# Performance work log

Hardware: AMD Instinct MI355X
Metric: run time of the kernel (lower is better)

## Reference

```python
import jax, jax.numpy as jnp
import numpy as np

N_HEAD, D_K = 16, 64  # from init_kwargs (d_v == d_k)

def setup_inputs() -> dict:
    key = jax.random.key(0)
    ks = jax.random.split(key, 8)
    B, S, D, DFF = 8, 1024, 1024, 4096
    s = 1.0 / np.sqrt(D)
    return {
        "enc_input": jax.random.normal(ks[0], (B, S, D), jnp.float32),
        "mask": jnp.ones((B, 1, S), jnp.int32),
        "gap": 1,
        "wq": jax.random.normal(ks[1], (D, N_HEAD * D_K), jnp.float32) * s,
        "wk": jax.random.normal(ks[2], (D, N_HEAD * D_K), jnp.float32) * s,
        "wv": jax.random.normal(ks[3], (D, N_HEAD * D_K), jnp.float32) * s,
        "wo": jax.random.normal(ks[4], (N_HEAD * D_K, D), jnp.float32) * s,
        "w1": jax.random.normal(ks[5], (D, DFF), jnp.float32) * s,
        "b1": jnp.zeros((DFF,), jnp.float32),
        "w2": jax.random.normal(ks[6], (DFF, D), jnp.float32) * (1.0 / np.sqrt(DFF)),
        "b2": jnp.zeros((D,), jnp.float32),
    }

def reference(enc_input, mask, gap, wq, wk, wv, wo, w1, b1, w2, b2):
    # dropout=0, use_layer_norm=0, adapter=0 are hard-coded in EncoderLayer.__init__
    B, S, D = enc_input.shape
    H, dk = N_HEAD, D_K
    temperature = dk ** 0.5

    q = (enc_input @ wq).reshape(B, S, H, dk).transpose(0, 2, 1, 3)  # [B,H,S,dk]
    k = (enc_input @ wk).reshape(B, S, H, dk).transpose(0, 2, 1, 3)
    v = (enc_input @ wv).reshape(B, S, H, dk).transpose(0, 2, 1, 3)

    attn = jnp.einsum('bhqd,bhkd->bhqk', q / temperature, k)  # [B,H,S,S]
    # mask [B,1,S] -> unsqueeze head dim -> [B,1,1,S]
    attn = jnp.where(mask[:, None] == 0, jnp.float32(-1e9), attn)
    attn = jax.nn.softmax(attn, axis=-1)

    ctx = jnp.einsum('bhqk,bhkd->bhqd', attn, v)          # [B,H,S,dk]
    ctx = ctx.transpose(0, 2, 1, 3).reshape(B, S, H * dk)  # [B,S,D]
    enc = ctx @ wo + enc_input                              # attn residual

    ffn = jax.nn.relu(enc @ w1 + b1) @ w2 + b2
    out = ffn + enc                                         # ffn residual
    return out, attn
```

## Files before the change

kernel.cpp:

```cpp
#include <hip/hip_runtime.h>
#include <hip/hip_bf16.h>
#include <stdint.h>

typedef __bf16 bf16x8 __attribute__((ext_vector_type(8)));
typedef float  f32x4  __attribute__((ext_vector_type(4)));

typedef __attribute__((address_space(1))) void gvoid;
typedef __attribute__((address_space(3))) void lvoid;

__device__ __forceinline__ void async16(void* lds, const void* g) {
    __builtin_amdgcn_global_load_lds((gvoid*)g, (lvoid*)lds, 16, 0, 0);
}

__device__ __forceinline__ float fexp2(float x) {
    return __builtin_amdgcn_exp2f(x);
}

__global__ void prep_all(const float* __restrict__ X, __hip_bfloat16* __restrict__ Xb,
                         const float* __restrict__ wq, const float* __restrict__ wk,
                         const float* __restrict__ wv, const float* __restrict__ wo,
                         const float* __restrict__ w1, const float* __restrict__ w2,
                         __hip_bfloat16* __restrict__ Wcat,
                         __hip_bfloat16* __restrict__ Wot,
                         __hip_bfloat16* __restrict__ W1t,
                         __hip_bfloat16* __restrict__ W2t) {
    const int tix = blockIdx.x;
    if (tix >= 12288) {
        const int bi = tix - 12288;
        const int tid = threadIdx.y * 32 + threadIdx.x;
        const long i = ((long)bi * 256 + tid) * 4;
        float4 v = *(const float4*)(X + i);
        __hip_bfloat162* d = (__hip_bfloat162*)(Xb + i);
        d[0] = __float22bfloat162_rn(make_float2(v.x, v.y));
        d[1] = __float22bfloat162_rn(make_float2(v.z, v.w));
        return;
    }
    __shared__ float t[32][33];
    const float* in;
    __hip_bfloat16* out;
    int R, C, cx, cy;
    if (tix < 4096) {
        int wid = tix >> 10, tile = tix & 1023;
        const float* srcs[4] = {wq, wk, wv, wo};
        __hip_bfloat16* dsts[4] = {Wcat, Wcat + 1024 * 1024, Wcat + 2 * 1024 * 1024, Wot};
        in = srcs[wid]; out = dsts[wid];
        R = 1024; C = 1024; cx = tile & 31; cy = tile >> 5;
    } else if (tix < 8192) {
        int tile = tix - 4096;
        in = w1; out = W1t; R = 1024; C = 4096;
        cx = tile & 127; cy = tile >> 7;
    } else {
        int tile = tix - 8192;
        in = w2; out = W2t; R = 4096; C = 1024;
        cx = tile & 31; cy = tile >> 5;
    }
    const int c0 = cx * 32, r0 = cy * 32;
    const int tx = threadIdx.x, ty = threadIdx.y;
#pragma unroll
    for (int i = 0; i < 4; ++i) {
        int r = r0 + ty + i * 8;
        t[ty + i * 8][tx] = in[(long)r * C + c0 + tx];
    }
    __syncthreads();
#pragma unroll
    for (int i = 0; i < 4; ++i) {
        int c = c0 + ty + i * 8;
        out[(long)c * R + r0 + tx] = __float2bfloat16(t[tx][ty + i * 8]);
    }
}

#define RBAR asm volatile("s_barrier" ::: "memory")

__global__ void __launch_bounds__(256, 2)
attn_fused(const __hip_bfloat16* __restrict__ QKb,
           const __hip_bfloat16* __restrict__ Vt,
           const int* __restrict__ mask,
           float* __restrict__ attn,
           __hip_bfloat16* __restrict__ Ctx) {
    __shared__ __align__(16) __hip_bfloat16 sK[128 * 64];
    __shared__ __align__(16) __hip_bfloat16 sV[64 * 128];
    __shared__ __align__(16) __hip_bfloat16 sP[128 * 128];
    __shared__ float smadd[1024];

    const int tid = threadIdx.x, lane = tid & 63, wave = tid >> 6;
    const int r16 = lane & 15, kg = lane >> 4;
    const float SC2 = 0.125f * 1.44269504f;

    const int dd = blockIdx.x;
    const int wgt = (dd & 7) * 128 + (dd >> 3);
    const int xblk = wgt & 7, z = wgt >> 3;
    const int b = z >> 4, h = z & 15;
    const int row0 = xblk * 128;
    const int wrow = wave * 32;

    const __hip_bfloat16* Qz = QKb + ((long)b * 1024 + row0) * 2048 + h * 64;
    const __hip_bfloat16* Kz = QKb + (long)b * 1024 * 2048 + 1024 + h * 64;
    const __hip_bfloat16* Vz = Vt + (long)z * 64 * 1024;
    float* attnZ = attn + (long)z * 1024 * 1024 + (long)row0 * 1024;

    for (int i = tid; i < 1024; i += 256)
        smadd[i] = mask[b * 1024 + i] ? 0.f : -1.5e9f;

    bf16x8 qa[2][2];
#pragma unroll
    for (int m = 0; m < 2; ++m)
#pragma unroll
        for (int kf = 0; kf < 2; ++kf)
            qa[m][kf] = *(const bf16x8*)(Qz + (long)(wrow + m * 16 + r16) * 2048 + kf * 32 + kg * 8);

    float lrow[2][4];
#pragma unroll
    for (int m = 0; m < 2; ++m)
#pragma unroll
        for (int i = 0; i < 4; ++i) lrow[m][i] = 0.f;

    const int ssw = (r16 & 7) << 4;

    auto stageK = [&](char* dst, int ct) {
#pragma unroll
        for (int j = 0; j < 4; ++j) {
            int c = wave * 4 + j;
            int s = c * 8 + (lane >> 3);
            int cb = (lane & 7) * 16;
            async16(dst + c * 1024,
                    (const char*)(Kz + (long)(ct * 128 + s) * 2048) + (cb ^ ((s & 7) << 4)));
        }
    };
    auto stageV = [&](int ct) {
#pragma unroll
        for (int j = 0; j < 4; ++j) {
            int c = wave * 4 + j;
            int dv = c * 4 + (lane >> 4);
            int cb = (lane & 15) * 16;
            async16((char*)sV + c * 1024,
                    (const char*)(Vz + (long)dv * 1024 + ct * 128) + (cb ^ ((dv & 7) << 4)));
        }
    };

    char* kbuf0 = (char*)sK;
    char* kbuf1 = (char*)sP;
    stageK(kbuf0, 0);

    for (int ct = 0; ct < 8; ++ct) {
        asm volatile("s_waitcnt vmcnt(0)" ::: "memory");
        __syncthreads();
        if (ct < 7) stageK((ct & 1) ? kbuf0 : kbuf1, ct + 1);
        const char* base = (ct & 1) ? kbuf1 : kbuf0;

        f32x4 sacc[2][8];
#pragma unroll
        for (int m = 0; m < 2; ++m)
#pragma unroll
            for (int nf = 0; nf < 8; ++nf) sacc[m][nf] = f32x4{0.f, 0.f, 0.f, 0.f};

        __builtin_amdgcn_s_setprio(1);
#pragma unroll
        for (int nf = 0; nf < 8; ++nf) {
            const char* kr = base + (nf * 16 + r16) * 128;
            bf16x8 bv0 = *(const bf16x8*)(kr + ((kg * 16) ^ ssw));
            bf16x8 bv1 = *(const bf16x8*)(kr + ((64 + kg * 16) ^ ssw));
#pragma unroll
            for (int m = 0; m < 2; ++m) {
                sacc[m][nf] = __builtin_amdgcn_mfma_f32_16x16x32_bf16(qa[m][0], bv0, sacc[m][nf], 0, 0, 0);
                sacc[m][nf] = __builtin_amdgcn_mfma_f32_16x16x32_bf16(qa[m][1], bv1, sacc[m][nf], 0, 0, 0);
            }
        }
        __builtin_amdgcn_s_setprio(0);

        float madd[8];
#pragma unroll
        for (int nf = 0; nf < 8; ++nf) madd[nf] = smadd[ct * 128 + nf * 16 + r16];

#pragma unroll
        for (int m = 0; m < 2; ++m)
#pragma unroll
            for (int i = 0; i < 4; ++i) {
                float ts = 0.f;
#pragma unroll
                for (int nf = 0; nf < 8; ++nf)
                    ts += fexp2(sacc[m][nf][i] * SC2 + madd[nf]);
#pragma unroll
                for (int o = 1; o < 16; o <<= 1) ts += __shfl_xor(ts, o);
                lrow[m][i] += ts;
            }
    }

    float rinv[2][4];
#pragma unroll
    for (int m = 0; m < 2; ++m)
#pragma unroll
        for (int i = 0; i < 4; ++i) rinv[m][i] = 1.0f / lrow[m][i];

    f32x4 oacc[2][4];
#pragma unroll
    for (int m = 0; m < 2; ++m)
#pragma unroll
        for (int nf = 0; nf < 4; ++nf) oacc[m][nf] = f32x4{0.f, 0.f, 0.f, 0.f};

    __syncthreads();
    stageK((char*)sK, 0);
    stageV(0);

    for (int ct = 0; ct < 8; ++ct) {
        asm volatile("s_waitcnt vmcnt(0)" ::: "memory");
        __syncthreads();

        f32x4 sacc[2][8];
#pragma unroll
        for (int m = 0; m < 2; ++m)
#pragma unroll
            for (int nf = 0; nf < 8; ++nf) sacc[m][nf] = f32x4{0.f, 0.f, 0.f, 0.f};

        __builtin_amdgcn_s_setprio(1);
#pragma unroll
        for (int nf = 0; nf < 8; ++nf) {
            const char* kr = (const char*)sK + (nf * 16 + r16) * 128;
            bf16x8 bv0 = *(const bf16x8*)(kr + ((kg * 16) ^ ssw));
            bf16x8 bv1 = *(const bf16x8*)(kr + ((64 + kg * 16) ^ ssw));
#pragma unroll
            for (int m = 0; m < 2; ++m) {
                sacc[m][nf] = __builtin_amdgcn_mfma_f32_16x16x32_bf16(qa[m][0], bv0, sacc[m][nf], 0, 0, 0);
                sacc[m][nf] = __builtin_amdgcn_mfma_f32_16x16x32_bf16(qa[m][1], bv1, sacc[m][nf], 0, 0, 0);
            }
        }
        __builtin_amdgcn_s_setprio(0);

        RBAR;
        if (ct < 7) stageK((char*)sK, ct + 1);

        float madd[8];
#pragma unroll
        for (int nf = 0; nf < 8; ++nf) madd[nf] = smadd[ct * 128 + nf * 16 + r16];

#pragma unroll
        for (int m = 0; m < 2; ++m)
#pragma unroll
            for (int nf = 0; nf < 8; ++nf) {
                int scol = nf * 16 + r16;
#pragma unroll
                for (int i = 0; i < 4; ++i) {
                    int q = wrow + m * 16 + kg * 4 + i;
                    float p = fexp2(sacc[m][nf][i] * SC2 + madd[nf]) * rinv[m][i];
                    __builtin_nontemporal_store(p, attnZ + (long)q * 1024 + ct * 128 + scol);
                    *(__hip_bfloat16*)((char*)sP + q * 256 + ((scol * 2) ^ ((q & 7) << 4))) =
                        __float2bfloat16(p);
                }
            }

        __builtin_amdgcn_s_setprio(1);
#pragma unroll
        for (int ks = 0; ks < 4; ++ks) {
            bf16x8 pa[2], vv[4];
#pragma unroll
            for (int m = 0; m < 2; ++m)
                pa[m] = *(const bf16x8*)((const char*)sP + (wrow + m * 16 + r16) * 256 +
                                         ((ks * 64 + kg * 16) ^ ssw));
#pragma unroll
            for (int nf = 0; nf < 4; ++nf)
                vv[nf] = *(const bf16x8*)((const char*)sV + (nf * 16 + r16) * 256 +
                                          ((ks * 64 + kg * 16) ^ ssw));
#pragma unroll
            for (int m = 0; m < 2; ++m)
#pragma unroll
                for (int nf = 0; nf < 4; ++nf)
                    oacc[m][nf] = __builtin_amdgcn_mfma_f32_16x16x32_bf16(pa[m], vv[nf], oacc[m][nf], 0, 0, 0);
        }
        __builtin_amdgcn_s_setprio(0);

        RBAR;
        if (ct < 7) stageV(ct + 1);
    }

#pragma unroll
    for (int m = 0; m < 2; ++m)
#pragma unroll
        for (int nf = 0; nf < 4; ++nf)
#pragma unroll
            for (int i = 0; i < 4; ++i) {
                int q = wrow + m * 16 + kg * 4 + i;
                Ctx[((long)b * 1024 + row0 + q) * 1024 + h * 64 + nf * 16 + r16] =
                    __float2bfloat16(oacc[m][nf][i]);
            }
}

#define RDA(BUF, PM, ML, KS) \
    (*(const bf16x8*)(aRd + (BUF)*32768 + (PM)*16384 + (ML)*2048 + ((((KS)*64) + kg*16) ^ sw)))
#define RDB(BUF, PN, NL, KS) \
    (*(const bf16x8*)(bRd + (BUF)*32768 + (PN)*16384 + (NL)*2048 + ((((KS)*64) + kg*16) ^ sw)))
#define LOAD_A(BUF, PM)                          \
    _Pragma("unroll") for (int ml = 0; ml < 4; ++ml) \
    _Pragma("unroll") for (int ks = 0; ks < 2; ++ks) \
        a[ml][ks] = RDA(BUF, PM, ml, ks)
#define LOAD_B(DST, BUF, PN)                     \
    _Pragma("unroll") for (int nl = 0; nl < 2; ++nl) \
    _Pragma("unroll") for (int ks = 0; ks < 2; ++ks) \
        DST[nl][ks] = RDB(BUF, PN, nl, ks)
#define MFMA16(PM, PN, BB)                                                   \
    __builtin_amdgcn_s_setprio(1);                                           \
    _Pragma("unroll") for (int ks = 0; ks < 2; ++ks)                         \
    _Pragma("unroll") for (int ml = 0; ml < 4; ++ml)                         \
    _Pragma("unroll") for (int nl = 0; nl < 2; ++nl)                         \
        acc[(PM)*4 + ml][(PN)*2 + nl] = __builtin_amdgcn_mfma_f32_16x16x32_bf16( \
            a[ml][ks], BB[nl][ks], acc[(PM)*4 + ml][(PN)*2 + nl], 0, 0, 0);  \
    __builtin_amdgcn_s_setprio(0)
#define BAR asm volatile("s_barrier" ::: "memory")

__global__ void __launch_bounds__(512, 2)
gemm256(const __hip_bfloat16* __restrict__ A, int lda,
        const __hip_bfloat16* __restrict__ Bt, int ldb,
        int K, int Mtiles,
        const float* __restrict__ bias, int relu,
        __hip_bfloat16* __restrict__ C, int ldc) {
    __shared__ __align__(16) char lds[131072];
    const int NT = K >> 6;
    const int tid = threadIdx.x, lane = tid & 63, wave = tid >> 6;
    const int r16 = lane & 15, kg = lane >> 4;
    const int wr = wave >> 2, wc = wave & 3;
    const int sw = (r16 & 7) << 4;

    const int nwg = gridDim.x;
    const int q8 = nwg >> 3, r8 = nwg & 7;
    const int xcd = blockIdx.x & 7, rest = blockIdx.x >> 3;
    const int wg = (xcd < r8 ? xcd * (q8 + 1) : r8 * (q8 + 1) + (xcd - r8) * q8) + rest;
    const int tm = wg % Mtiles, tn = wg / Mtiles;
    const long row0 = (long)tm * 256, col0 = (long)tn * 256;

    const int idx = tid >> 3;
    const int slotp = ((tid & 7) ^ (idx & 7)) * 8;
    const __hip_bfloat16* aSrc[4];
    const __hip_bfloat16* bSrc[4];
#pragma unroll
    for (int j = 0; j < 4; ++j) {
        long ar = row0 + (j & 1) * 128 + (j >> 1) * 64 + idx;
        aSrc[j] = A + ar * lda + slotp;
        long br = col0 + ((j & 1) * 2 + (tid >> 8)) * 64 + (j >> 1) * 32 + (idx & 31);
        bSrc[j] = Bt + br * ldb + slotp;
    }

    char* ldsA = lds;
    char* ldsB = lds + 65536;
    const int stDst = wave * 1024;
    auto stA = [&](int v, int j) {
        async16(ldsA + ((v & 1) << 15) + (j << 13) + stDst, aSrc[j] + (v << 6));
    };
    auto stB = [&](int v, int j) {
        async16(ldsB + ((v & 1) << 15) + (j << 13) + stDst, bSrc[j] + (v << 6));
    };

    stA(0, 0); stA(0, 1); stB(0, 0); stB(0, 1);
    stA(0, 2); stA(0, 3); stB(0, 2); stB(0, 3);
    stA(1, 0); stA(1, 1); stB(1, 0); stB(1, 1);
    asm volatile("s_waitcnt vmcnt(4)" ::: "memory");
    BAR;

    f32x4 acc[8][4] = {};
    const char* aRd = ldsA + wr * 8192 + r16 * 128;
    const char* bRd = ldsB + wc * 4096 + r16 * 128;

    for (int u = 0; u < NT; u += 2) {
        const bool more = (u + 2) < NT;
        bf16x8 a[4][2], b0[2][2], b1[2][2];

        LOAD_A(0, 0);
        LOAD_B(b0, 0, 0);
        stA(u + 1, 2); stA(u + 1, 3);
        MFMA16(0, 0, b0);
        BAR;

        LOAD_B(b1, 0, 1);
        stB(u + 1, 2); stB(u + 1, 3);
        MFMA16(0, 1, b1);
        BAR;

        LOAD_A(0, 1);
        if (more) { stA(u + 2, 0); stA(u + 2, 1); }
        MFMA16(1, 0, b0);
        BAR;

        if (more) {
            stB(u + 2, 0); stB(u + 2, 1);
            asm volatile("s_waitcnt vmcnt(4)" ::: "memory");
        } else {
            asm volatile("s_waitcnt vmcnt(0)" ::: "memory");
        }
        MFMA16(1, 1, b1);
        BAR;

        LOAD_A(1, 0);
        LOAD_B(b0, 1, 0);
        if (more) { stA(u + 2, 2); stA(u + 2, 3); }
        MFMA16(0, 0, b0);
        BAR;

        LOAD_B(b1, 1, 1);
        if (more) { stB(u + 2, 2); stB(u + 2, 3); }
        MFMA16(0, 1, b1);
        BAR;

        LOAD_A(1, 1);
        if (more) { stA(u + 3, 0); stA(u + 3, 1); }
        MFMA16(1, 0, b0);
        BAR;

        if (more) {
            stB(u + 3, 0); stB(u + 3, 1);
            asm volatile("s_waitcnt vmcnt(4)" ::: "memory");
        }
        MFMA16(1, 1, b1);
        BAR;
    }

    const long crow = row0 + wr * 128, ccol = col0 + wc * 64;
#pragma unroll
    for (int mf = 0; mf < 8; ++mf)
#pragma unroll
        for (int nf = 0; nf < 4; ++nf) {
            const long col = ccol + nf * 16 + r16;
            const float bs = bias ? bias[col] : 0.f;
#pragma unroll
            for (int i = 0; i < 4; ++i) {
                const long row = crow + mf * 16 + kg * 4 + i;
                float v = acc[mf][nf][i] + bs;
                if (relu) v = fmaxf(v, 0.f);
                C[row * (long)ldc + col] = __float2bfloat16(v);
            }
        }
}

#define RDB128(BUF, NL, KS) \
    (*(const bf16x8*)(bRd + (BUF)*16384 + (NL)*2048 + ((((KS)*64) + kg*16) ^ sw)))
#define LOAD_B128(DST, BUF)                      \
    _Pragma("unroll") for (int nl = 0; nl < 2; ++nl) \
    _Pragma("unroll") for (int ks = 0; ks < 2; ++ks) \
        DST[nl][ks] = RDB128(BUF, nl, ks)
#define MFMA16N(PM, BB)                                                      \
    __builtin_amdgcn_s_setprio(1);                                           \
    _Pragma("unroll") for (int ks = 0; ks < 2; ++ks)                         \
    _Pragma("unroll") for (int ml = 0; ml < 4; ++ml)                         \
    _Pragma("unroll") for (int nl = 0; nl < 2; ++nl)                         \
        acc[(PM)*4 + ml][nl] = __builtin_amdgcn_mfma_f32_16x16x32_bf16(      \
            a[ml][ks], BB[nl][ks], acc[(PM)*4 + ml][nl], 0, 0, 0);           \
    __builtin_amdgcn_s_setprio(0)

__global__ void __launch_bounds__(512, 2)
gemm256n128(const __hip_bfloat16* __restrict__ A, int lda,
            const __hip_bfloat16* __restrict__ Bt, int ldb,
            int K, int Mtiles,
            const float* __restrict__ bias, int relu,
            const float* __restrict__ resf,
            const __hip_bfloat16* __restrict__ resb, int ldres,
            float* __restrict__ Cf, __hip_bfloat16* __restrict__ Cb, int ldc) {
    __shared__ __align__(16) char lds[98304];
    const int NT = K >> 6;
    const int tid = threadIdx.x, lane = tid & 63, wave = tid >> 6;
    const int r16 = lane & 15, kg = lane >> 4;
    const int wr = wave >> 2, wc = wave & 3;
    const int sw = (r16 & 7) << 4;

    const int nwg = gridDim.x;
    const int q8 = nwg >> 3, r8 = nwg & 7;
    const int xcd = blockIdx.x & 7, rest = blockIdx.x >> 3;
    const int wg = (xcd < r8 ? xcd * (q8 + 1) : r8 * (q8 + 1) + (xcd - r8) * q8) + rest;
    const int tm = wg % Mtiles, tn = wg / Mtiles;
    const long row0 = (long)tm * 256, col0 = (long)tn * 128;

    const int idx = tid >> 3;
    const int slotp = ((tid & 7) ^ (idx & 7)) * 8;
    const __hip_bfloat16* aSrc[4];
    const __hip_bfloat16* bSrc[2];
#pragma unroll
    for (int j = 0; j < 4; ++j) {
        long ar = row0 + (j & 1) * 128 + (j >> 1) * 64 + idx;
        aSrc[j] = A + ar * lda + slotp;
    }
#pragma unroll
    for (int j = 0; j < 2; ++j) {
        long br = col0 + j * 64 + idx;
        bSrc[j] = Bt + br * ldb + slotp;
    }

    char* ldsA = lds;
    char* ldsB = lds + 65536;
    const int stDst = wave * 1024;
    auto stA = [&](int v, int j) {
        async16(ldsA + ((v & 1) << 15) + (j << 13) + stDst, aSrc[j] + (v << 6));
    };
    auto stB = [&](int v, int j) {
        async16(ldsB + ((v & 1) << 14) + (j << 13) + stDst, bSrc[j] + (v << 6));
    };

    stA(0, 0); stA(0, 1); stA(0, 2); stA(0, 3);
    stB(0, 0); stB(0, 1);
    stA(1, 0); stA(1, 1);
    stB(1, 0); stB(1, 1);
    asm volatile("s_waitcnt vmcnt(4)" ::: "memory");
    BAR;

    f32x4 acc[8][2] = {};
    const char* aRd = ldsA + wr * 8192 + r16 * 128;
    const char* bRd = ldsB + wc * 4096 + r16 * 128;

    for (int u = 0; u < NT; u += 2) {
        const bool more = (u + 2) < NT;
        bf16x8 a[4][2], b0[2][2], b1[2][2];

        LOAD_A(0, 0);
        LOAD_B128(b0, 0);
        stA(u + 1, 2); stA(u + 1, 3);
        MFMA16N(0, b0);
        BAR;

        LOAD_A(0, 1);
        if (more) {
            stA(u + 2, 0); stA(u + 2, 1);
            stB(u + 2, 0); stB(u + 2, 1);
            asm volatile("s_waitcnt vmcnt(4)" ::: "memory");
        } else {
            asm volatile("s_waitcnt vmcnt(0)" ::: "memory");
        }
        MFMA16N(1, b0);
        BAR;

        LOAD_A(1, 0);
        LOAD_B128(b1, 1);
        if (more) { stA(u + 2, 2); stA(u + 2, 3); }
        MFMA16N(0, b1);
        BAR;

        LOAD_A(1, 1);
        if (more) {
            stA(u + 3, 0); stA(u + 3, 1);
            stB(u + 3, 0); stB(u + 3, 1);
            asm volatile("s_waitcnt vmcnt(4)" ::: "memory");
        }
        MFMA16N(1, b1);
        BAR;
    }

    const long crow = row0 + wr * 128, ccol = col0 + wc * 32;
#pragma unroll
    for (int mf = 0; mf < 8; ++mf)
#pragma unroll
        for (int nf = 0; nf < 2; ++nf) {
            const long col = ccol + nf * 16 + r16;
            const float bs = bias ? bias[col] : 0.f;
#pragma unroll
            for (int i = 0; i < 4; ++i) {
                const long row = crow + mf * 16 + kg * 4 + i;
                float v = acc[mf][nf][i] + bs;
                if (relu) v = fmaxf(v, 0.f);
                if (resf) v += resf[row * (long)ldres + col];
                if (resb) v += __bfloat162float(resb[row * (long)ldres + col]);
                const long off = row * (long)ldc + col;
                if (Cf) Cf[off] = v;
                if (Cb) Cb[off] = __float2bfloat16(v);
            }
        }
}

__global__ void __launch_bounds__(512, 2)
gemm_v(const __hip_bfloat16* __restrict__ A, int lda,
       const __hip_bfloat16* __restrict__ Bt, int ldb,
       int K,
       __hip_bfloat16* __restrict__ Vt) {
    __shared__ __align__(16) char lds[98304];
    const int NT = K >> 6;
    const int tid = threadIdx.x, lane = tid & 63, wave = tid >> 6;
    const int r16 = lane & 15, kg = lane >> 4;
    const int wr = wave >> 2, wc = wave & 3;
    const int sw = (r16 & 7) << 4;

    const int nwg = gridDim.x;
    const int q8 = nwg >> 3, r8 = nwg & 7;
    const int xcd = blockIdx.x & 7, rest = blockIdx.x >> 3;
    const int wg = (xcd < r8 ? xcd * (q8 + 1) : r8 * (q8 + 1) + (xcd - r8) * q8) + rest;
    const int tm = wg & 31, tn = wg >> 5;
    const long row0 = (long)tm * 256, col0 = (long)tn * 128;

    const int idx = tid >> 3;
    const int slotp = ((tid & 7) ^ (idx & 7)) * 8;
    const __hip_bfloat16* aSrc[4];
    const __hip_bfloat16* bSrc[2];
#pragma unroll
    for (int j = 0; j < 4; ++j) {
        long ar = row0 + (j & 1) * 128 + (j >> 1) * 64 + idx;
        aSrc[j] = A + ar * lda + slotp;
    }
#pragma unroll
    for (int j = 0; j < 2; ++j) {
        long br = col0 + j * 64 + idx;
        bSrc[j] = Bt + br * ldb + slotp;
    }

    char* ldsA = lds;
    char* ldsB = lds + 65536;
    const int stDst = wave * 1024;
    auto stA = [&](int v, int j) {
        async16(ldsA + ((v & 1) << 15) + (j << 13) + stDst, aSrc[j] + (v << 6));
    };
    auto stB = [&](int v, int j) {
        async16(ldsB + ((v & 1) << 14) + (j << 13) + stDst, bSrc[j] + (v << 6));
    };

    stA(0, 0); stA(0, 1); stA(0, 2); stA(0, 3);
    stB(0, 0); stB(0, 1);
    stA(1, 0); stA(1, 1);
    stB(1, 0); stB(1, 1);
    asm volatile("s_waitcnt vmcnt(4)" ::: "memory");
    BAR;

    f32x4 acc[8][2] = {};
    const char* aRd = ldsA + wr * 8192 + r16 * 128;
    const char* bRd = ldsB + wc * 4096 + r16 * 128;

    for (int u = 0; u < NT; u += 2) {
        const bool more = (u + 2) < NT;
        bf16x8 a[4][2], b0[2][2], b1[2][2];

        LOAD_A(0, 0);
        LOAD_B128(b0, 0);
        stA(u + 1, 2); stA(u + 1, 3);
        MFMA16N(0, b0);
        BAR;

        LOAD_A(0, 1);
        if (more) {
            stA(u + 2, 0); stA(u + 2, 1);
            stB(u + 2, 0); stB(u + 2, 1);
            asm volatile("s_waitcnt vmcnt(4)" ::: "memory");
        } else {
            asm volatile("s_waitcnt vmcnt(0)" ::: "memory");
        }
        MFMA16N(1, b0);
        BAR;

        LOAD_A(1, 0);
        LOAD_B128(b1, 1);
        if (more) { stA(u + 2, 2); stA(u + 2, 3); }
        MFMA16N(0, b1);
        BAR;

        LOAD_A(1, 1);
        if (more) {
            stA(u + 3, 0); stA(u + 3, 1);
            stB(u + 3, 0); stB(u + 3, 1);
            asm volatile("s_waitcnt vmcnt(4)" ::: "memory");
        }
        MFMA16N(1, b1);
        BAR;
    }

    __hip_bfloat16* sT = (__hip_bfloat16*)lds;
    {
        const int cls = wc * 32;
        const int rls = wr * 128 + kg * 4;
#pragma unroll
        for (int mf = 0; mf < 8; ++mf)
#pragma unroll
            for (int nf = 0; nf < 2; ++nf) {
                int cl = cls + nf * 16 + r16;
                int rl = rls + mf * 16;
                __hip_bfloat162 lo = __float22bfloat162_rn(make_float2(acc[mf][nf][0], acc[mf][nf][1]));
                __hip_bfloat162 hi = __float22bfloat162_rn(make_float2(acc[mf][nf][2], acc[mf][nf][3]));
                *(__hip_bfloat162*)(&sT[cl * 264 + rl]) = lo;
                *(__hip_bfloat162*)(&sT[cl * 264 + rl + 2]) = hi;
            }
    }
    __syncthreads();
    {
        const int b = (int)(row0 >> 10);
        const int s_base = (int)(row0 & 1023);
#pragma unroll
        for (int j = 0; j < 8; ++j) {
            int dl = wave * 16 + j * 2 + (lane >> 5);
            int sc = (lane & 31) * 8;
            bf16x8 v = *(const bf16x8*)(&sT[dl * 264 + sc]);
            int dg = (int)col0 + dl;
            int z = b * 16 + (dg >> 6);
            int d = dg & 63;
            *(bf16x8*)(Vt + ((long)z * 64 + d) * 1024 + s_base + sc) = v;
        }
    }
}

extern "C" void kernel_launch(void* const* d_in, const int* in_sizes, int n_in,
                              void* d_out, int out_size, void* d_ws, size_t ws_size,
                              hipStream_t stream) {
    const int B = 8, S = 1024, D = 1024, DFF = 4096;
    const long SD = (long)B * S * D;

    const float* X  = (const float*)d_in[0];
    const int*  msk = (const int*)d_in[1];
    const float* wq = (const float*)d_in[3];
    const float* wk = (const float*)d_in[4];
    const float* wv = (const float*)d_in[5];
    const float* wo = (const float*)d_in[6];
    const float* w1 = (const float*)d_in[7];
    const float* b1 = (const float*)d_in[8];
    const float* w2 = (const float*)d_in[9];
    const float* b2 = (const float*)d_in[10];

    float* out  = (float*)d_out;
    float* attn = out + SD;

    char* ws = (char*)d_ws;
    auto alloc = [&](size_t bytes) {
        char* p = ws;
        ws += (bytes + 255) & ~(size_t)255;
        return p;
    };
    __hip_bfloat16* Xb   = (__hip_bfloat16*)alloc(SD * 2);
    __hip_bfloat16* QKb  = (__hip_bfloat16*)alloc(SD * 4);
    __hip_bfloat16* Vt   = (__hip_bfloat16*)alloc(SD * 2);
    __hip_bfloat16* Ctx  = (__hip_bfloat16*)alloc(SD * 2);
    __hip_bfloat16* EncB = (__hip_bfloat16*)alloc(SD * 2);
    __hip_bfloat16* Hb   = (__hip_bfloat16*)alloc((long)B * S * DFF * 2);
    __hip_bfloat16* Wcat = (__hip_bfloat16*)alloc((long)3 * D * D * 2);
    __hip_bfloat16* Wot  = (__hip_bfloat16*)alloc((long)D * D * 2);
    __hip_bfloat16* W1t  = (__hip_bfloat16*)alloc((long)D * DFF * 2);
    __hip_bfloat16* W2t  = (__hip_bfloat16*)alloc((long)D * DFF * 2);
    (void)ws_size; (void)in_sizes; (void)n_in; (void)out_size;

    dim3 tb(32, 8);
    prep_all<<<dim3(12288 + 8192), tb, 0, stream>>>(X, Xb, wq, wk, wv, wo, w1, w2,
                                                    Wcat, Wot, W1t, W2t);

    gemm256<<<dim3(32 * 8), 512, 0, stream>>>(
        Xb, D, Wcat, D, D, 32, nullptr, 0, QKb, 2048);

    gemm_v<<<dim3(32 * 8), 512, 0, stream>>>(
        Xb, D, Wcat + (long)2048 * 1024, D, D, Vt);

    attn_fused<<<dim3(1024), 256, 0, stream>>>(QKb, Vt, msk, attn, Ctx);

    gemm256n128<<<dim3(32 * 8), 512, 0, stream>>>(
        Ctx, D, Wot, D, D, 32,
        nullptr, 0, X, nullptr, D,
        nullptr, EncB, D);

    gemm256<<<dim3(32 * 16), 512, 0, stream>>>(
        EncB, D, W1t, D, D, 32, b1, 1, Hb, DFF);

    gemm256n128<<<dim3(32 * 8), 512, 0, stream>>>(
        Hb, DFF, W2t, DFF, DFF, 32,
        b2, 0, nullptr, EncB, D,
        out, nullptr, D);
}
```

Measured before the change: 510.4 us.

## Double-buffer V tiles and split P×V into halves in the attention pass

The second attention pass now double-buffers the V tile in LDS and issues the next K and V loads together, right after the QK^T MFMAs. The softmax-write and P·V step is split into two halves, so the P staging buffer shrinks to half its size and one loop-top barrier goes away. The goal is to overlap V loading with the exponent/store work and to cut synchronisation per tile. The end-of-iteration wait is only vmcnt(63), which may not guarantee the prefetched tiles have landed, especially with many outstanding nontemporal stores. That makes correctness depend on timing.

```diff
diff --git a/kernel.cpp b/kernel.cpp
--- a/kernel.cpp
+++ b/kernel.cpp
@@ -78,8 +78,8 @@
            float* __restrict__ attn,
            __hip_bfloat16* __restrict__ Ctx) {
     __shared__ __align__(16) __hip_bfloat16 sK[128 * 64];
-    __shared__ __align__(16) __hip_bfloat16 sV[64 * 128];
-    __shared__ __align__(16) __hip_bfloat16 sP[128 * 128];
+    __shared__ __align__(16) __hip_bfloat16 sV[2][64 * 128];
+    __shared__ __align__(16) __hip_bfloat16 sP[128 * 64];
     __shared__ float smadd[1024];
 
     const int tid = threadIdx.x, lane = tid & 63, wave = tid >> 6;
@@ -126,13 +126,13 @@
                     (const char*)(Kz + (long)(ct * 128 + s) * 2048) + (cb ^ ((s & 7) << 4)));
         }
     };
-    auto stageV = [&](int ct) {
+    auto stageV = [&](int ct, int buf) {
 #pragma unroll
         for (int j = 0; j < 4; ++j) {
             int c = wave * 4 + j;
             int dv = c * 4 + (lane >> 4);
             int cb = (lane & 15) * 16;
-            async16((char*)sV + c * 1024,
+            async16((char*)sV[buf] + c * 1024,
                     (const char*)(Vz + (long)dv * 1024 + ct * 128) + (cb ^ ((dv & 7) << 4)));
         }
     };
@@ -199,12 +199,11 @@
 
     __syncthreads();
     stageK((char*)sK, 0);
-    stageV(0);
+    stageV(0, 0);
+    asm volatile("s_waitcnt vmcnt(0)" ::: "memory");
+    __syncthreads();
 
     for (int ct = 0; ct < 8; ++ct) {
-        asm volatile("s_waitcnt vmcnt(0)" ::: "memory");
-        __syncthreads();
-
         f32x4 sacc[2][8];
 #pragma unroll
         for (int m = 0; m < 2; ++m)
@@ -226,49 +225,63 @@
         __builtin_amdgcn_s_setprio(0);
 
         RBAR;
-        if (ct < 7) stageK((char*)sK, ct + 1);
+        if (ct < 7) {
+            stageK((char*)sK, ct + 1);
+            stageV(ct + 1, (ct + 1) & 1);
+        }
+        asm volatile("" ::: "memory");
 
         float madd[8];
 #pragma unroll
         for (int nf = 0; nf < 8; ++nf) madd[nf] = smadd[ct * 128 + nf * 16 + r16];
 
-#pragma unroll
-        for (int m = 0; m < 2; ++m)
-#pragma unroll
-            for (int nf = 0; nf < 8; ++nf) {
-                int scol = nf * 16 + r16;
-#pragma unroll
-                for (int i = 0; i < 4; ++i) {
-                    int q = wrow + m * 16 + kg * 4 + i;
-                    float p = fexp2(sacc[m][nf][i] * SC2 + madd[nf]) * rinv[m][i];
-                    __builtin_nontemporal_store(p, attnZ + (long)q * 1024 + ct * 128 + scol);
-                    *(__hip_bfloat16*)((char*)sP + q * 256 + ((scol * 2) ^ ((q & 7) << 4))) =
-                        __float2bfloat16(p);
+        const char* sVb = (const char*)sV[ct & 1];
+
+#pragma unroll
+        for (int half = 0; half < 2; ++half) {
+#pragma unroll
+            for (int m = 0; m < 2; ++m)
+#pragma unroll
+                for (int nf = 0; nf < 4; ++nf) {
+                    const int nfg = half * 4 + nf;
+                    const int scol = nfg * 16 + r16;
+                    const int scl = nf * 16 + r16;
+#pragma unroll
+                    for (int i = 0; i < 4; ++i) {
+                        int q = wrow + m * 16 + kg * 4 + i;
+                        float p = fexp2(sacc[m][nfg][i] * SC2 + madd[nfg]) * rinv[m][i];
+                        __builtin_nontemporal_store(p, attnZ + (long)q * 1024 + ct * 128 + scol);
+                        *(__hip_bfloat16*)((char*)sP + q * 128 + ((scl * 2) ^ ((q & 7) << 4))) =
+                            __float2bfloat16(p);
+                    }
                 }
+
+            __builtin_amdgcn_s_setprio(1);
+#pragma unroll
+            for (int ks = 0; ks < 2; ++ks) {
+                const int ksg = half * 2 + ks;
+                bf16x8 pa[2], vv[4];
+#pragma unroll
+                for (int m = 0; m < 2; ++m)
+                    pa[m] = *(const bf16x8*)((const char*)sP + (wrow + m * 16 + r16) * 128 +
+                                             ((ks * 64 + kg * 16) ^ ssw));
+#pragma unroll
+                for (int nf = 0; nf < 4; ++nf)
+                    vv[nf] = *(const bf16x8*)(sVb + (nf * 16 + r16) * 256 +
+                                              ((ksg * 64 + kg * 16) ^ ssw));
+#pragma unroll
+                for (int m = 0; m < 2; ++m)
+#pragma unroll
+                    for (int nf = 0; nf < 4; ++nf)
+                        oacc[m][nf] = __builtin_amdgcn_mfma_f32_16x16x32_bf16(pa[m], vv[nf], oacc[m][nf], 0, 0, 0);
             }
-
-        __builtin_amdgcn_s_setprio(1);
-#pragma unroll
-        for (int ks = 0; ks < 4; ++ks) {
-            bf16x8 pa[2], vv[4];
-#pragma unroll
-            for (int m = 0; m < 2; ++m)
-                pa[m] = *(const bf16x8*)((const char*)sP + (wrow + m * 16 + r16) * 256 +
-                                         ((ks * 64 + kg * 16) ^ ssw));
-#pragma unroll
-            for (int nf = 0; nf < 4; ++nf)
-                vv[nf] = *(const bf16x8*)((const char*)sV + (nf * 16 + r16) * 256 +
-                                          ((ks * 64 + kg * 16) ^ ssw));
-#pragma unroll
-            for (int m = 0; m < 2; ++m)
-#pragma unroll
-                for (int nf = 0; nf < 4; ++nf)
-                    oacc[m][nf] = __builtin_amdgcn_mfma_f32_16x16x32_bf16(pa[m], vv[nf], oacc[m][nf], 0, 0, 0);
-        }
-        __builtin_amdgcn_s_setprio(0);
-
-        RBAR;
-        if (ct < 7) stageV(ct + 1);
+            __builtin_amdgcn_s_setprio(0);
+        }
+
+        if (ct < 7) {
+            asm volatile("s_waitcnt vmcnt(63)" ::: "memory");
+            RBAR;
+        }
     }
 
 #pragma unroll
```

After: 500.8 us. About the same (-1.9%).
